# Optimization experiments

Measured on AMD Instinct MI355X. Metric: run time of the kernel, lower is better.

## Reference

```python
import jax, jax.numpy as jnp
import numpy as np
import math

B, S, D, H = 8, 1024, 1024, 16
DH = D // H  # 64


def setup_inputs() -> dict:
    key = jax.random.key(0)
    ks = jax.random.split(key, 10)
    inputs = jax.random.normal(ks[0], (B, S, D), dtype=jnp.float32)
    mask = jax.random.randint(ks[1], (B, S, S), 0, 2) == 1  # bool [B,S,S]
    sc = 1.0 / math.sqrt(D)
    # per-head projection weights stacked: [H, D, DH], biases [H, DH]
    Wq = jax.random.normal(ks[2], (H, D, DH), dtype=jnp.float32) * sc
    bq = jax.random.normal(ks[3], (H, DH), dtype=jnp.float32) * 0.02
    Wk = jax.random.normal(ks[4], (H, D, DH), dtype=jnp.float32) * sc
    bk = jax.random.normal(ks[5], (H, DH), dtype=jnp.float32) * 0.02
    Wv = jax.random.normal(ks[6], (H, D, DH), dtype=jnp.float32) * sc
    bv = jax.random.normal(ks[7], (H, DH), dtype=jnp.float32) * 0.02
    Wo = jax.random.normal(ks[8], (D, D), dtype=jnp.float32) * sc
    bo = jax.random.normal(ks[9], (D,), dtype=jnp.float32) * 0.02
    return {"inputs": inputs, "mask": mask, "Wq": Wq, "bq": bq, "Wk": Wk,
            "bk": bk, "Wv": Wv, "bv": bv, "Wo": Wo, "bo": bo}


def reference(inputs, mask, Wq, bq, Wk, bk, Wv, bv, Wo, bo):
    d_model = inputs.shape[-1]
    scale = 1.0 / jnp.sqrt(jnp.asarray(d_model, inputs.dtype))  # note: sqrt(d_model), as in source
    # batched per-head projections: [B,H,S,DH]
    Q = jnp.einsum('bsd,hde->bhse', inputs, Wq) + bq[None, :, None, :]
    K = jnp.einsum('bsd,hde->bhse', inputs, Wk) + bk[None, :, None, :]
    V = jnp.einsum('bsd,hde->bhse', inputs, Wv) + bv[None, :, None, :]
    scores = jnp.einsum('bhse,bhte->bhst', Q, K) * scale  # [B,H,S,S]
    scores = jnp.where(mask[:, None, :, :], jnp.asarray(-1e9, scores.dtype), scores)
    attn = jax.nn.softmax(scores, axis=-1)
    ctx = jnp.einsum('bhst,bhte->bhse', attn, V)  # [B,H,S,DH]
    # concat heads along last dim (head h -> slice h*DH:(h+1)*DH), matches torch.cat
    bsz, h, s, dh = ctx.shape
    x = ctx.transpose(0, 2, 1, 3).reshape(bsz, s, h * dh)
    return x @ Wo + bo
```

## Files before the change

### kernel.cpp

```cpp
#include <hip/hip_runtime.h>
#include <hip/hip_bf16.h>
#include <stdint.h>


typedef __attribute__((ext_vector_type(8))) short short8;
typedef __attribute__((ext_vector_type(4))) float floatx4;

#define C2S 0.04508422f

__device__ __forceinline__ int swz(int r, int kc) { return r * 8 + (kc ^ (r & 7)); }
__device__ __forceinline__ short8 as_frag(uint4 u) { return __builtin_bit_cast(short8, u); }
__device__ __forceinline__ floatx4 mfma16(short8 a, short8 b, floatx4 c) {
    return __builtin_amdgcn_mfma_f32_16x16x32_bf16(a, b, c, 0, 0, 0);
}
__device__ __forceinline__ unsigned short f2bu(float f) {
    return __builtin_bit_cast(unsigned short, __float2bfloat16(f));
}
__device__ __forceinline__ short f2b(float f) {
    return __builtin_bit_cast(short, __float2bfloat16(f));
}
__device__ __forceinline__ float b2f(short s) {
    return __bfloat162float(__builtin_bit_cast(__hip_bfloat16, s));
}
__device__ __forceinline__ void dma16(const void* g, void* l) {
    __builtin_amdgcn_global_load_lds(
        (const __attribute__((address_space(1))) uint32_t*)g,
        (__attribute__((address_space(3))) uint32_t*)l, 16, 0, 0);
}
__device__ __forceinline__ uint2 pack4(float a, float b, float c, float d) {
    uint2 p;
    p.x = (unsigned)f2bu(a) | ((unsigned)f2bu(b) << 16);
    p.y = (unsigned)f2bu(c) | ((unsigned)f2bu(d) << 16);
    return p;
}

__device__ __forceinline__ void detect_mode(const unsigned* Xw, int* s_is32) {
    if (threadIdx.x < 64) {
        unsigned lo = Xw[threadIdx.x] & 0xFFFFu;
        unsigned e = (lo >> 7) & 0xFFu;
        unsigned long long bal = __ballot(e >= 88u && e <= 150u);
        if (threadIdx.x == 0) *s_is32 = (bal != ~0ull) ? 1 : 0;
    }
    __syncthreads();
}

__device__ __forceinline__ float load_elt(const void* p, size_t idx, int is32) {
    return is32 ? ((const float*)p)[idx]
                : __bfloat162float(((const __hip_bfloat16*)p)[idx]);
}

__global__ __launch_bounds__(256) void prep_all(
    const void* __restrict__ Wq, const void* __restrict__ Wk,
    const void* __restrict__ Wv, const void* __restrict__ Wo,
    const void* __restrict__ bq, const void* __restrict__ bk,
    const void* __restrict__ bv, const void* __restrict__ bo,
    const void* __restrict__ mask_raw, const void* __restrict__ X,
    __hip_bfloat16* __restrict__ WT, __hip_bfloat16* __restrict__ WoT,
    __hip_bfloat16* __restrict__ bc, unsigned long long* __restrict__ bits64,
    __hip_bfloat16* __restrict__ Xb, int do_x)
{
    __shared__ __hip_bfloat16 T[64][72];
    __shared__ int s_is32;
    int blk = blockIdx.x;
    int tid = threadIdx.x;
    const unsigned* Xw = (const unsigned*)X;

    if (blk < 1024) {
        detect_mode(Xw, &s_is32);
        const void* src; size_t src_off;
        __hip_bfloat16* dst;
        int src_ld, dst_ld;
        if (blk < 768) {
            int p = blk >> 8;
            int rem = blk & 255;
            int h = rem >> 4, dt = rem & 15;
            src = (p == 0) ? Wq : (p == 1) ? Wk : Wv;
            src_off = ((size_t)h * 1024 + (size_t)dt * 64) * 64;
            dst = WT + (((size_t)p * 16 + h) * 64) * 1024 + dt * 64;
            src_ld = 64; dst_ld = 1024;
        } else {
            int t = blk - 768;
            int kt = t >> 4, nt = t & 15;
            src = Wo; src_off = (size_t)kt * 64 * 1024 + nt * 64;
            dst = WoT + (size_t)nt * 64 * 1024 + kt * 64;
            src_ld = 1024; dst_ld = 1024;
        }
        #pragma unroll
        for (int i = 0; i < 2; i++) {
            int seg = tid + i * 256;
            int r = seg >> 3, c0 = (seg & 7) * 8;
            if (s_is32) {
                const float* sf = (const float*)src + src_off + (size_t)r * src_ld + c0;
                float4 f0 = *(const float4*)sf;
                float4 f1 = *(const float4*)(sf + 4);
                T[c0 + 0][r] = __float2bfloat16(f0.x);
                T[c0 + 1][r] = __float2bfloat16(f0.y);
                T[c0 + 2][r] = __float2bfloat16(f0.z);
                T[c0 + 3][r] = __float2bfloat16(f0.w);
                T[c0 + 4][r] = __float2bfloat16(f1.x);
                T[c0 + 5][r] = __float2bfloat16(f1.y);
                T[c0 + 6][r] = __float2bfloat16(f1.z);
                T[c0 + 7][r] = __float2bfloat16(f1.w);
            } else {
                const __hip_bfloat16* sh =
                    (const __hip_bfloat16*)src + src_off + (size_t)r * src_ld + c0;
                uint4 u = *(const uint4*)sh;
                short8 s8 = __builtin_bit_cast(short8, u);
                #pragma unroll
                for (int j = 0; j < 8; j++)
                    T[c0 + j][r] = __builtin_bit_cast(__hip_bfloat16, (short)s8[j]);
            }
        }
        __syncthreads();
        #pragma unroll
        for (int i = 0; i < 2; i++) {
            int seg = tid + i * 256;
            int r = seg >> 3, c0 = (seg & 7) * 8;
            *(uint4*)(dst + (size_t)r * dst_ld + c0) = *(const uint4*)(&T[r][c0]);
        }
    } else if (blk == 1024) {
        detect_mode(Xw, &s_is32);
        #pragma unroll
        for (int i = 0; i < 16; i++) {
            int idx = tid + i * 256;
            int which = idx >> 10, j = idx & 1023;
            const void* src = (which == 0) ? bq : (which == 1) ? bk : (which == 2) ? bv : bo;
            float v = load_elt(src, j, s_is32);
            if (which == 0) v *= C2S;
            bc[idx] = __float2bfloat16(v);
        }
    } else if (blk < 2561) {
        int blkL = blk - 1025;
        const int* mi = (const int*)mask_raw;
        const unsigned char* mb = (const unsigned char*)mask_raw;
        int lane = tid & 63;
        bool ok = true;
        #pragma unroll
        for (int i = 0; i < 4; i++) {
            unsigned v = (unsigned)mi[lane * 4 + i];
            if (v > 1u) ok = false;
        }
        bool is_i32 = (__ballot(ok) == ~0ull);
        int gw = (blkL * 256 + tid) >> 6;
        const int NW = 1536 * 4;
        const int NWORDS = (8 * 1024 * 1024) / 64;
        if (is_i32) {
            for (int i = gw; i < NWORDS; i += NW) {
                int mv = mi[(size_t)i * 64 + lane];
                unsigned long long bal = __ballot(mv != 0);
                if (lane == 0) {
                    int bb = i >> 14, q = (i >> 4) & 1023, t = i & 15;
                    bits64[((size_t)bb << 14) + ((size_t)t << 10) + q] = bal;
                }
            }
        } else {
            for (int i = gw; i < NWORDS; i += NW) {
                int mv = mb[(size_t)i * 64 + lane];
                unsigned long long bal = __ballot(mv != 0);
                if (lane == 0) {
                    int bb = i >> 14, q = (i >> 4) & 1023, t = i & 15;
                    bits64[((size_t)bb << 14) + ((size_t)t << 10) + q] = bal;
                }
            }
        }
    } else if (do_x) {
        detect_mode(Xw, &s_is32);
        int blkL = blk - 2561;
        size_t g = ((size_t)blkL * 256 + tid) * 16;
        if (s_is32) {
            const float* Xf = (const float*)X;
            #pragma unroll
            for (int half = 0; half < 2; half++) {
                float4 f0 = *(const float4*)(Xf + g + half * 8);
                float4 f1 = *(const float4*)(Xf + g + half * 8 + 4);
                short8 s;
                s[0] = f2b(f0.x); s[1] = f2b(f0.y); s[2] = f2b(f0.z); s[3] = f2b(f0.w);
                s[4] = f2b(f1.x); s[5] = f2b(f1.y); s[6] = f2b(f1.z); s[7] = f2b(f1.w);
                *(uint4*)(Xb + g + half * 8) = __builtin_bit_cast(uint4, s);
            }
        } else {
            const uint4* Xu = (const uint4*)X;
            *(uint4*)(Xb + g)     = Xu[g / 8];
            *(uint4*)(Xb + g + 8) = Xu[g / 8 + 1];
        }
    }
}

__global__ __launch_bounds__(256, 2) void qkv_gemm_dma(
    const __hip_bfloat16* __restrict__ Xb,
    const __hip_bfloat16* __restrict__ WT,
    const __hip_bfloat16* __restrict__ bc,
    __hip_bfloat16* __restrict__ Q,
    __hip_bfloat16* __restrict__ Ko,
    __hip_bfloat16* __restrict__ Vt)
{
    __shared__ uint4 AsU[256 * 8];
    __shared__ uint4 BsU[128 * 8];
    int tid = threadIdx.x, lane = tid & 63, wave = tid >> 6;
    int quad = lane >> 4, ln = lane & 15;
    int mw = wave & 1, nw = wave >> 1;
    int m0 = blockIdx.x * 256;
    int n0 = blockIdx.y * 128;
    const __hip_bfloat16* Wp = WT + (size_t)n0 * 1024;

    floatx4 acc[8][4];
    #pragma unroll
    for (int i = 0; i < 8; i++)
        #pragma unroll
        for (int j = 0; j < 4; j++) acc[i][j] = (floatx4){0.f, 0.f, 0.f, 0.f};

    for (int k0 = 0; k0 < 1024; k0 += 64) {
        #pragma unroll
        for (int i = 0; i < 8; i++) {
            int r = wave * 64 + i * 8 + (lane >> 3);
            int kc = (lane & 7) ^ (r & 7);
            char* lds = (char*)AsU + (size_t)(wave * 512 + i * 64) * 16;
            dma16(Xb + (size_t)(m0 + r) * 1024 + k0 + kc * 8, lds);
        }
        #pragma unroll
        for (int i = 0; i < 4; i++) {
            int r = wave * 32 + i * 8 + (lane >> 3);
            int kc = (lane & 7) ^ (r & 7);
            char* lds = (char*)BsU + (size_t)(wave * 256 + i * 64) * 16;
            dma16(Wp + (size_t)r * 1024 + k0 + kc * 8, lds);
        }
        __syncthreads();
        #pragma unroll
        for (int kk = 0; kk < 2; kk++) {
            short8 af[8], bf[4];
            #pragma unroll
            for (int mi = 0; mi < 8; mi++)
                af[mi] = as_frag(AsU[swz(mw * 128 + mi * 16 + ln, kk * 4 + quad)]);
            #pragma unroll
            for (int ni = 0; ni < 4; ni++)
                bf[ni] = as_frag(BsU[swz(nw * 64 + ni * 16 + ln, kk * 4 + quad)]);
            #pragma unroll
            for (int mi = 0; mi < 8; mi++)
                #pragma unroll
                for (int ni = 0; ni < 4; ni++)
                    acc[mi][ni] = mfma16(af[mi], bf[ni], acc[mi][ni]);
        }
        __syncthreads();
    }

    int b = m0 >> 10;
    int s0 = m0 & 1023;
    int proj = n0 >> 10;
    if (proj == 2) {
        #pragma unroll
        for (int ni = 0; ni < 4; ni++) {
            int n = n0 + nw * 64 + ni * 16 + ln;
            int h = (n >> 6) & 15, e = n & 63;
            float bval = __bfloat162float(bc[2 * 1024 + (n & 1023)]);
            #pragma unroll
            for (int mi = 0; mi < 8; mi++) {
                int sb = s0 + mw * 128 + mi * 16 + quad * 4;
                uint2 pk = pack4(acc[mi][ni][0] + bval, acc[mi][ni][1] + bval,
                                 acc[mi][ni][2] + bval, acc[mi][ni][3] + bval);
                *(uint2*)(Vt + (((size_t)b * 16 + h) * 64 + e) * 1024 + sb) = pk;
            }
        }
    } else {
        __hip_bfloat16* P = (proj == 0) ? Q : Ko;
        float sc = (proj == 0) ? C2S : 1.f;
        #pragma unroll
        for (int ni = 0; ni < 4; ni++) {
            int n = n0 + nw * 64 + ni * 16 + ln;
            int h = (n >> 6) & 15, e = n & 63;
            float bval = __bfloat162float(bc[proj * 1024 + (n & 1023)]);
            #pragma unroll
            for (int mi = 0; mi < 8; mi++) {
                #pragma unroll
                for (int r = 0; r < 4; r++) {
                    int s = s0 + mw * 128 + mi * 16 + quad * 4 + r;
                    P[(((size_t)b * 16 + h) * 1024 + s) * 64 + e] =
                        __float2bfloat16(acc[mi][ni][r] * sc + bval);
                }
            }
        }
    }
}

__global__ __launch_bounds__(256) void qkv_gemm2(
    const void* __restrict__ Xsrc,
    const __hip_bfloat16* __restrict__ WT,
    const __hip_bfloat16* __restrict__ bc,
    __hip_bfloat16* __restrict__ Q,
    __hip_bfloat16* __restrict__ Ko,
    __hip_bfloat16* __restrict__ Vt)
{
    __shared__ int s_is32;
    detect_mode((const unsigned*)Xsrc, &s_is32);
    __shared__ uint4 AsU[128 * 8];
    __shared__ uint4 BsU[128 * 8];
    int tid = threadIdx.x, lane = tid & 63, wave = tid >> 6;
    int quad = lane >> 4, ln = lane & 15;
    int m0 = blockIdx.x * 128;
    int n0 = blockIdx.y * 128;
    const __hip_bfloat16* Wp = WT + (size_t)n0 * 1024;
    const float* Xf = (const float*)Xsrc;
    const __hip_bfloat16* Xh = (const __hip_bfloat16*)Xsrc;

    floatx4 acc[2][8];
    #pragma unroll
    for (int i = 0; i < 2; i++)
        #pragma unroll
        for (int j = 0; j < 8; j++) acc[i][j] = (floatx4){0.f, 0.f, 0.f, 0.f};

    for (int k0 = 0; k0 < 1024; k0 += 64) {
        if (s_is32) {
            #pragma unroll
            for (int i = 0; i < 4; i++) {
                int id = tid + i * 256;
                int r = id >> 3, kc = id & 7;
                size_t off = (size_t)(m0 + r) * 1024 + k0 + kc * 8;
                float4 f0 = *(const float4*)(Xf + off);
                float4 f1 = *(const float4*)(Xf + off + 4);
                short8 s;
                s[0] = f2b(f0.x); s[1] = f2b(f0.y); s[2] = f2b(f0.z); s[3] = f2b(f0.w);
                s[4] = f2b(f1.x); s[5] = f2b(f1.y); s[6] = f2b(f1.z); s[7] = f2b(f1.w);
                AsU[swz(r, kc)] = __builtin_bit_cast(uint4, s);
            }
        } else {
            #pragma unroll
            for (int i = 0; i < 4; i++) {
                int id = tid + i * 256;
                int r = id >> 3, kc = id & 7;
                AsU[swz(r, kc)] = *(const uint4*)(Xh + (size_t)(m0 + r) * 1024 + k0 + kc * 8);
            }
        }
        #pragma unroll
        for (int i = 0; i < 4; i++) {
            int id = tid + i * 256;
            int r = id >> 3, kc = id & 7;
            BsU[swz(r, kc)] = *(const uint4*)(Wp + (size_t)r * 1024 + k0 + kc * 8);
        }
        __syncthreads();
        #pragma unroll
        for (int kk = 0; kk < 2; kk++) {
            short8 a0 = as_frag(AsU[swz(wave * 32 + ln, kk * 4 + quad)]);
            short8 a1 = as_frag(AsU[swz(wave * 32 + 16 + ln, kk * 4 + quad)]);
            #pragma unroll
            for (int nt = 0; nt < 8; nt++) {
                short8 bf = as_frag(BsU[swz(nt * 16 + ln, kk * 4 + quad)]);
                acc[0][nt] = mfma16(a0, bf, acc[0][nt]);
                acc[1][nt] = mfma16(a1, bf, acc[1][nt]);
            }
        }
        __syncthreads();
    }

    int b = m0 >> 10;
    int s0 = m0 & 1023;
    #pragma unroll
    for (int nt = 0; nt < 8; nt++) {
        int n = n0 + nt * 16 + ln;
        int proj = n >> 10, h = (n >> 6) & 15, e = n & 63;
        float bval = __bfloat162float(bc[proj * 1024 + (n & 1023)]);
        float sc = (proj == 0) ? C2S : 1.f;
        #pragma unroll
        for (int mt = 0; mt < 2; mt++) {
            #pragma unroll
            for (int r = 0; r < 4; r++) {
                int s = s0 + wave * 32 + mt * 16 + quad * 4 + r;
                float v = acc[mt][nt][r] * sc + bval;
                if (proj == 2) {
                    Vt[(((size_t)b * 16 + h) * 64 + e) * 1024 + s] = __float2bfloat16(v);
                } else {
                    __hip_bfloat16* P = (proj == 0) ? Q : Ko;
                    P[(((size_t)b * 16 + h) * 1024 + s) * 64 + e] = __float2bfloat16(v);
                }
            }
        }
    }
}

__global__ __launch_bounds__(512, 4) void attn(
    const __hip_bfloat16* __restrict__ Q,
    const __hip_bfloat16* __restrict__ K,
    const __hip_bfloat16* __restrict__ Vt,
    const unsigned long long* __restrict__ bits,
    __hip_bfloat16* __restrict__ ctx)
{
    __shared__ uint4 KsU[2 * 512];
    __shared__ uint4 VsU[2 * 512];
    __shared__ uint4 PsU[8 * 256];

    int tid = threadIdx.x, lane = tid & 63, w = tid >> 6;
    int quad = lane >> 4, ln = lane & 15;
    int bh = blockIdx.x;
    int q0 = blockIdx.y * 256;
    int b = bh >> 4, h = bh & 15;
    const __hip_bfloat16* Qp = Q + (size_t)bh * 1024 * 64;
    const __hip_bfloat16* Kp = K + (size_t)bh * 1024 * 64;
    const __hip_bfloat16* Vp = Vt + (size_t)bh * 64 * 1024;
    const unsigned long long* bp = bits + (size_t)b * 16 * 1024;

    short8 qf[2][2];
    #pragma unroll
    for (int g = 0; g < 2; g++)
        #pragma unroll
        for (int kk = 0; kk < 2; kk++)
            qf[g][kk] = as_frag(*(const uint4*)(
                Qp + (size_t)(q0 + w * 32 + g * 16 + ln) * 64 + kk * 32 + quad * 8));

    int r8 = lane >> 3;
    int kc = (lane & 7) ^ r8;

    floatx4 acc_o[2][4];
    #pragma unroll
    for (int g = 0; g < 2; g++)
        #pragma unroll
        for (int i = 0; i < 4; i++) acc_o[g][i] = (floatx4){0.f, 0.f, 0.f, 0.f};
    float lsum[2] = {0.f, 0.f};
    __hip_bfloat16* Pw = (__hip_bfloat16*)&PsU[w * 256];

    for (int t0 = 0; t0 < 1024; t0 += 128) {
        __syncthreads();
        int t64b = t0 >> 6;
        unsigned long long m00 = bp[((size_t)t64b << 10) + q0 + w * 32 + ln];
        unsigned long long m01 = bp[((size_t)t64b << 10) + q0 + w * 32 + 16 + ln];
        unsigned long long m10 = bp[((size_t)(t64b + 1) << 10) + q0 + w * 32 + ln];
        unsigned long long m11 = bp[((size_t)(t64b + 1) << 10) + q0 + w * 32 + 16 + ln];
        #pragma unroll
        for (int i = 0; i < 2; i++) {
            int tK = t0 + i * 64 + w * 8 + r8;
            dma16(Kp + (size_t)tK * 64 + kc * 8,
                  (char*)KsU + (size_t)(i * 512 + w * 64) * 16);
            int e = w * 8 + r8;
            dma16(Vp + (size_t)e * 1024 + t0 + i * 64 + kc * 8,
                  (char*)VsU + (size_t)(i * 512 + w * 64) * 16);
        }
        __syncthreads();

        #pragma unroll
        for (int s = 0; s < 2; s++) {
            unsigned long long mcur0 = s ? m10 : m00;
            unsigned long long mcur1 = s ? m11 : m01;
            const uint4* Ks = KsU + s * 512;
            const uint4* Vs = VsU + s * 512;

            floatx4 st[2][4];
            #pragma unroll
            for (int g = 0; g < 2; g++)
                #pragma unroll
                for (int i = 0; i < 4; i++) st[g][i] = (floatx4){0.f, 0.f, 0.f, 0.f};
            __builtin_amdgcn_s_setprio(1);
            #pragma unroll
            for (int kk = 0; kk < 2; kk++) {
                #pragma unroll
                for (int tt = 0; tt < 4; tt++) {
                    short8 kf = as_frag(Ks[swz(tt * 16 + ln, kk * 4 + quad)]);
                    st[0][tt] = mfma16(kf, qf[0][kk], st[0][tt]);
                    st[1][tt] = mfma16(kf, qf[1][kk], st[1][tt]);
                }
            }
            __builtin_amdgcn_s_setprio(0);

            #pragma unroll
            for (int g = 0; g < 2; g++) {
                int qloc = g * 16 + ln;
                unsigned long long msh = (g ? mcur1 : mcur0) >> (quad * 4);
                #pragma unroll
                for (int tt = 0; tt < 4; tt++) {
                    unsigned mb = (unsigned)(msh >> (tt * 16)) & 0xFu;
                    float pe0 = (mb & 1u) ? 0.f : __builtin_amdgcn_exp2f(st[g][tt][0]);
                    float pe1 = (mb & 2u) ? 0.f : __builtin_amdgcn_exp2f(st[g][tt][1]);
                    float pe2 = (mb & 4u) ? 0.f : __builtin_amdgcn_exp2f(st[g][tt][2]);
                    float pe3 = (mb & 8u) ? 0.f : __builtin_amdgcn_exp2f(st[g][tt][3]);
                    lsum[g] += (pe0 + pe1) + (pe2 + pe3);
                    int kcp = tt * 2 + (quad >> 1);
                    int off = qloc * 64 + (kcp ^ (qloc & 7)) * 8 + (quad & 1) * 4;
                    *(uint2*)(Pw + off) = pack4(pe0, pe1, pe2, pe3);
                }
            }

            __builtin_amdgcn_s_setprio(1);
            #pragma unroll
            for (int kk = 0; kk < 2; kk++) {
                short8 pf0 = as_frag(PsU[w * 256 + swz(0 * 16 + ln, kk * 4 + quad)]);
                short8 pf1 = as_frag(PsU[w * 256 + swz(1 * 16 + ln, kk * 4 + quad)]);
                #pragma unroll
                for (int et = 0; et < 4; et++) {
                    short8 vf = as_frag(Vs[swz(et * 16 + ln, kk * 4 + quad)]);
                    acc_o[0][et] = mfma16(vf, pf0, acc_o[0][et]);
                    acc_o[1][et] = mfma16(vf, pf1, acc_o[1][et]);
                }
            }
            __builtin_amdgcn_s_setprio(0);
        }
    }

    #pragma unroll
    for (int g = 0; g < 2; g++) {
        lsum[g] += __shfl_xor(lsum[g], 16, 64);
        lsum[g] += __shfl_xor(lsum[g], 32, 64);
    }

    #pragma unroll
    for (int g = 0; g < 2; g++) {
        float inv = 1.f / fmaxf(lsum[g], 1e-20f);
        int s = q0 + w * 32 + g * 16 + ln;
        __hip_bfloat16* crow = ctx + ((size_t)b * 1024 + s) * 1024 + h * 64 + quad * 4;
        #pragma unroll
        for (int et = 0; et < 4; et++) {
            uint2 pk = pack4(acc_o[g][et][0] * inv, acc_o[g][et][1] * inv,
                             acc_o[g][et][2] * inv, acc_o[g][et][3] * inv);
            *(uint2*)(crow + et * 16) = pk;
        }
    }
}

__global__ __launch_bounds__(256) void out_gemm_dma(
    const __hip_bfloat16* __restrict__ Cx,
    const __hip_bfloat16* __restrict__ WoT,
    const __hip_bfloat16* __restrict__ bc,
    const unsigned* __restrict__ Xw,
    void* __restrict__ dout,
    int direct)
{
    __shared__ int s_is32;
    detect_mode(Xw, &s_is32);
    __shared__ uint4 AsU[128 * 8];
    __shared__ uint4 BsU[128 * 8];
    int tid = threadIdx.x, lane = tid & 63, wave = tid >> 6;
    int quad = lane >> 4, ln = lane & 15;
    int mw = wave & 1, nw = wave >> 1;
    int m0 = blockIdx.x * 128;
    int n0 = blockIdx.y * 128;

    floatx4 acc[4][4];
    #pragma unroll
    for (int i = 0; i < 4; i++)
        #pragma unroll
        for (int j = 0; j < 4; j++) acc[i][j] = (floatx4){0.f, 0.f, 0.f, 0.f};

    for (int k0 = 0; k0 < 1024; k0 += 64) {
        #pragma unroll
        for (int i = 0; i < 4; i++) {
            int r = wave * 32 + i * 8 + (lane >> 3);
            int kc = (lane & 7) ^ (r & 7);
            char* ldsA = (char*)AsU + (size_t)(wave * 256 + i * 64) * 16;
            char* ldsB = (char*)BsU + (size_t)(wave * 256 + i * 64) * 16;
            dma16(Cx + (size_t)(m0 + r) * 1024 + k0 + kc * 8, ldsA);
            dma16(WoT + (size_t)(n0 + r) * 1024 + k0 + kc * 8, ldsB);
        }
        __syncthreads();
        #pragma unroll
        for (int kk = 0; kk < 2; kk++) {
            short8 af[4], bf[4];
            #pragma unroll
            for (int mi = 0; mi < 4; mi++)
                af[mi] = as_frag(AsU[swz(mw * 64 + mi * 16 + ln, kk * 4 + quad)]);
            #pragma unroll
            for (int ni = 0; ni < 4; ni++)
                bf[ni] = as_frag(BsU[swz(nw * 64 + ni * 16 + ln, kk * 4 + quad)]);
            #pragma unroll
            for (int mi = 0; mi < 4; mi++)
                #pragma unroll
                for (int ni = 0; ni < 4; ni++)
                    acc[mi][ni] = mfma16(af[mi], bf[ni], acc[mi][ni]);
        }
        __syncthreads();
    }

    const __hip_bfloat16* bo = bc + 3 * 1024;
    #pragma unroll
    for (int ni = 0; ni < 4; ni++) {
        int n = n0 + nw * 64 + ni * 16 + ln;
        float bval = __bfloat162float(bo[n]);
        #pragma unroll
        for (int mi = 0; mi < 4; mi++) {
            #pragma unroll
            for (int r = 0; r < 4; r++) {
                int m = m0 + mw * 64 + mi * 16 + quad * 4 + r;
                float v = acc[mi][ni][r] + bval;
                if (direct && s_is32) ((float*)dout)[(size_t)m * 1024 + n] = v;
                else ((__hip_bfloat16*)dout)[(size_t)m * 1024 + n] = __float2bfloat16(v);
            }
        }
    }
}

__global__ __launch_bounds__(256) void emit_out(
    const __hip_bfloat16* __restrict__ Fo, const unsigned* __restrict__ Xw,
    void* __restrict__ dout)
{
    __shared__ int s_is32;
    detect_mode(Xw, &s_is32);
    size_t g = (size_t)blockIdx.x * 256 + threadIdx.x;
    uint4 u = *(const uint4*)(Fo + g * 8);
    if (s_is32) {
        short8 s = __builtin_bit_cast(short8, u);
        float4 f0, f1;
        f0.x = b2f(s[0]); f0.y = b2f(s[1]); f0.z = b2f(s[2]); f0.w = b2f(s[3]);
        f1.x = b2f(s[4]); f1.y = b2f(s[5]); f1.z = b2f(s[6]); f1.w = b2f(s[7]);
        *(float4*)((float*)dout + g * 8) = f0;
        *(float4*)((float*)dout + g * 8 + 4) = f1;
    } else {
        *(uint4*)((__hip_bfloat16*)dout + g * 8) = u;
    }
}

extern "C" void kernel_launch(void* const* d_in, const int* in_sizes, int n_in,
                              void* d_out, int out_size, void* d_ws, size_t ws_size,
                              hipStream_t stream) {
    const void* X  = d_in[0];
    const void* mk = d_in[1];
    const void* Wq = d_in[2];
    const void* bq = d_in[3];
    const void* Wk = d_in[4];
    const void* bk = d_in[5];
    const void* Wv = d_in[6];
    const void* bv = d_in[7];
    const void* Wo = d_in[8];
    const void* bo = d_in[9];
    const unsigned* Xw = (const unsigned*)X;

    char* ws = (char*)d_ws;
    __hip_bfloat16*     WT   = (__hip_bfloat16*)(ws);
    __hip_bfloat16*     WoT  = (__hip_bfloat16*)(ws + ((size_t)6 << 20));
    unsigned long long* bits = (unsigned long long*)(ws + ((size_t)8 << 20));
    __hip_bfloat16*     bc   = (__hip_bfloat16*)(ws + ((size_t)9 << 20));
    __hip_bfloat16*     Xb   = (__hip_bfloat16*)(ws + ((size_t)10 << 20));
    __hip_bfloat16*     Qb   = (__hip_bfloat16*)(ws + ((size_t)26 << 20));
    __hip_bfloat16*     Kb   = (__hip_bfloat16*)(ws + ((size_t)42 << 20));
    __hip_bfloat16*     Vtb  = (__hip_bfloat16*)(ws + ((size_t)58 << 20));

    bool bigws = ws_size >= ((size_t)74 << 20);

    hipLaunchKernelGGL(prep_all, dim3(4609), dim3(256), 0, stream,
                       Wq, Wk, Wv, Wo, bq, bk, bv, bo, mk, X,
                       WT, WoT, bc, bits, Xb, bigws ? 1 : 0);

    if (bigws) {
        __hip_bfloat16* Cx = Xb;
        hipLaunchKernelGGL(qkv_gemm_dma, dim3(32, 24), dim3(256), 0, stream,
                           Xb, WT, bc, Qb, Kb, Vtb);
        hipLaunchKernelGGL(attn, dim3(128, 4), dim3(512), 0, stream,
                           Qb, Kb, Vtb, bits, Cx);
        hipLaunchKernelGGL(out_gemm_dma, dim3(64, 8), dim3(256), 0, stream,
                           Cx, WoT, bc, Xw, d_out, 1);
    } else {
        __hip_bfloat16* Cx = (__hip_bfloat16*)d_out;
        __hip_bfloat16* Fo = Qb;
        hipLaunchKernelGGL(qkv_gemm2, dim3(64, 24), dim3(256), 0, stream,
                           X, WT, bc, Qb, Kb, Vtb);
        hipLaunchKernelGGL(attn, dim3(128, 4), dim3(512), 0, stream,
                           Qb, Kb, Vtb, bits, Cx);
        hipLaunchKernelGGL(out_gemm_dma, dim3(64, 8), dim3(256), 0, stream,
                           Cx, WoT, bc, Xw, (void*)Fo, 0);
        hipLaunchKernelGGL(emit_out, dim3(4096), dim3(256), 0, stream,
                           Fo, Xw, d_out);
    }
}
```

Before: 289.6 us.

## Pipeline QKV GEMM with double-buffered async loads and 256x256 tiles

Rewrites the QKV projection GEMM to use 512-thread blocks computing 256x256 tiles. The K dimension is split into 32-wide half-stages that are double-buffered in LDS. Async global-to-LDS copies for upcoming stages are issued between MFMA phases, gated by explicit vmcnt waits and raw barriers, and s_setprio raises the MFMA issue priority. The goal is to overlap memory traffic with matrix math and halve the number of B-tile reloads. In exchange the kernel uses 128KB of LDS, which lowers occupancy, and relies on hand-placed wait counts being correct.

```diff
diff --git a/kernel.cpp b/kernel.cpp
--- a/kernel.cpp
+++ b/kernel.cpp
@@ -186,7 +186,48 @@
     }
 }
 
-__global__ __launch_bounds__(256, 2) void qkv_gemm_dma(
+#define VM6 asm volatile("s_waitcnt vmcnt(6)" ::: "memory")
+#define VM0 asm volatile("s_waitcnt vmcnt(0)" ::: "memory")
+#define FENCE asm volatile("" ::: "memory")
+
+#define QPH(BUF, KK, MH, LOADB, STAGE_STMT, WAIT_STMT)                          \
+  {                                                                             \
+    const int base_ = ((BUF) * 2 + (KK)) * 1024;                                \
+    short8 af0 = as_frag(AsU[base_ + (mw * 128 + ((MH) * 4 + 0) * 16 + ln) * 4 + rslot]); \
+    short8 af1 = as_frag(AsU[base_ + (mw * 128 + ((MH) * 4 + 1) * 16 + ln) * 4 + rslot]); \
+    short8 af2 = as_frag(AsU[base_ + (mw * 128 + ((MH) * 4 + 2) * 16 + ln) * 4 + rslot]); \
+    short8 af3 = as_frag(AsU[base_ + (mw * 128 + ((MH) * 4 + 3) * 16 + ln) * 4 + rslot]); \
+    if (LOADB) {                                                                \
+      bf[0] = as_frag(BsU[base_ + (nw * 64 + 0 * 16 + ln) * 4 + rslot]);        \
+      bf[1] = as_frag(BsU[base_ + (nw * 64 + 1 * 16 + ln) * 4 + rslot]);        \
+      bf[2] = as_frag(BsU[base_ + (nw * 64 + 2 * 16 + ln) * 4 + rslot]);        \
+      bf[3] = as_frag(BsU[base_ + (nw * 64 + 3 * 16 + ln) * 4 + rslot]);        \
+    }                                                                           \
+    STAGE_STMT;                                                                 \
+    FENCE; __builtin_amdgcn_s_barrier(); FENCE;                                 \
+    __builtin_amdgcn_s_setprio(1);                                              \
+    acc[(MH) * 4 + 0][0] = mfma16(af0, bf[0], acc[(MH) * 4 + 0][0]);            \
+    acc[(MH) * 4 + 0][1] = mfma16(af0, bf[1], acc[(MH) * 4 + 0][1]);            \
+    acc[(MH) * 4 + 0][2] = mfma16(af0, bf[2], acc[(MH) * 4 + 0][2]);            \
+    acc[(MH) * 4 + 0][3] = mfma16(af0, bf[3], acc[(MH) * 4 + 0][3]);            \
+    acc[(MH) * 4 + 1][0] = mfma16(af1, bf[0], acc[(MH) * 4 + 1][0]);            \
+    acc[(MH) * 4 + 1][1] = mfma16(af1, bf[1], acc[(MH) * 4 + 1][1]);            \
+    acc[(MH) * 4 + 1][2] = mfma16(af1, bf[2], acc[(MH) * 4 + 1][2]);            \
+    acc[(MH) * 4 + 1][3] = mfma16(af1, bf[3], acc[(MH) * 4 + 1][3]);            \
+    acc[(MH) * 4 + 2][0] = mfma16(af2, bf[0], acc[(MH) * 4 + 2][0]);            \
+    acc[(MH) * 4 + 2][1] = mfma16(af2, bf[1], acc[(MH) * 4 + 2][1]);            \
+    acc[(MH) * 4 + 2][2] = mfma16(af2, bf[2], acc[(MH) * 4 + 2][2]);            \
+    acc[(MH) * 4 + 2][3] = mfma16(af2, bf[3], acc[(MH) * 4 + 2][3]);            \
+    acc[(MH) * 4 + 3][0] = mfma16(af3, bf[0], acc[(MH) * 4 + 3][0]);            \
+    acc[(MH) * 4 + 3][1] = mfma16(af3, bf[1], acc[(MH) * 4 + 3][1]);            \
+    acc[(MH) * 4 + 3][2] = mfma16(af3, bf[2], acc[(MH) * 4 + 3][2]);            \
+    acc[(MH) * 4 + 3][3] = mfma16(af3, bf[3], acc[(MH) * 4 + 3][3]);            \
+    __builtin_amdgcn_s_setprio(0);                                              \
+    WAIT_STMT;                                                                  \
+    FENCE; __builtin_amdgcn_s_barrier(); FENCE;                                 \
+  }
+
+__global__ __launch_bounds__(512, 2) void qkv_gemm_dma(
     const __hip_bfloat16* __restrict__ Xb,
     const __hip_bfloat16* __restrict__ WT,
     const __hip_bfloat16* __restrict__ bc,
@@ -194,53 +235,63 @@
     __hip_bfloat16* __restrict__ Ko,
     __hip_bfloat16* __restrict__ Vt)
 {
-    __shared__ uint4 AsU[256 * 8];
-    __shared__ uint4 BsU[128 * 8];
-    int tid = threadIdx.x, lane = tid & 63, wave = tid >> 6;
+    __shared__ uint4 AsU[4096];
+    __shared__ uint4 BsU[4096];
+    int tid = threadIdx.x, lane = tid & 63, w = tid >> 6;
     int quad = lane >> 4, ln = lane & 15;
-    int mw = wave & 1, nw = wave >> 1;
+    int mw = w & 1, nw = w >> 1;
     int m0 = blockIdx.x * 256;
-    int n0 = blockIdx.y * 128;
+    int n0 = blockIdx.y * 256;
     const __hip_bfloat16* Wp = WT + (size_t)n0 * 1024;
 
+    int l2 = lane >> 2;
+    int kcS = (lane & 3) ^ (l2 & 3);
+    int rslot = quad ^ (ln & 3);
+
     floatx4 acc[8][4];
     #pragma unroll
     for (int i = 0; i < 8; i++)
         #pragma unroll
         for (int j = 0; j < 4; j++) acc[i][j] = (floatx4){0.f, 0.f, 0.f, 0.f};
 
-    for (int k0 = 0; k0 < 1024; k0 += 64) {
-        #pragma unroll
-        for (int i = 0; i < 8; i++) {
-            int r = wave * 64 + i * 8 + (lane >> 3);
-            int kc = (lane & 7) ^ (r & 7);
-            char* lds = (char*)AsU + (size_t)(wave * 512 + i * 64) * 16;
-            dma16(Xb + (size_t)(m0 + r) * 1024 + k0 + kc * 8, lds);
-        }
-        #pragma unroll
-        for (int i = 0; i < 4; i++) {
-            int r = wave * 32 + i * 8 + (lane >> 3);
-            int kc = (lane & 7) ^ (r & 7);
-            char* lds = (char*)BsU + (size_t)(wave * 256 + i * 64) * 16;
-            dma16(Wp + (size_t)r * 1024 + k0 + kc * 8, lds);
-        }
-        __syncthreads();
-        #pragma unroll
-        for (int kk = 0; kk < 2; kk++) {
-            short8 af[8], bf[4];
-            #pragma unroll
-            for (int mi = 0; mi < 8; mi++)
-                af[mi] = as_frag(AsU[swz(mw * 128 + mi * 16 + ln, kk * 4 + quad)]);
-            #pragma unroll
-            for (int ni = 0; ni < 4; ni++)
-                bf[ni] = as_frag(BsU[swz(nw * 64 + ni * 16 + ln, kk * 4 + quad)]);
-            #pragma unroll
-            for (int mi = 0; mi < 8; mi++)
-                #pragma unroll
-                for (int ni = 0; ni < 4; ni++)
-                    acc[mi][ni] = mfma16(af[mi], bf[ni], acc[mi][ni]);
-        }
-        __syncthreads();
+    auto stA = [&](int kt, int kh) {
+        int kh2 = (kt & 1) * 2 + kh;
+        #pragma unroll
+        for (int j = 0; j < 2; j++) {
+            int r = (w * 2 + j) * 16 + l2;
+            dma16(Xb + (size_t)(m0 + r) * 1024 + kt * 64 + kh * 32 + kcS * 8,
+                  (char*)AsU + (size_t)(kh2 * 1024 + (w * 2 + j) * 64) * 16);
+        }
+    };
+    auto stB = [&](int kt, int kh) {
+        int kh2 = (kt & 1) * 2 + kh;
+        #pragma unroll
+        for (int j = 0; j < 2; j++) {
+            int r = (w * 2 + j) * 16 + l2;
+            dma16(Wp + (size_t)r * 1024 + kt * 64 + kh * 32 + kcS * 8,
+                  (char*)BsU + (size_t)(kh2 * 1024 + (w * 2 + j) * 64) * 16);
+        }
+    };
+
+    stB(0, 0); stA(0, 0); stB(0, 1); stA(0, 1);
+    stB(1, 0); stA(1, 0); stB(1, 1);
+    VM6;
+    FENCE; __builtin_amdgcn_s_barrier(); FENCE;
+
+    short8 bf[4];
+    for (int it = 0; it < 8; it++) {
+        int T = 2 * it;
+        bool more = (it < 7);
+        QPH(0, 0, 0, 1, { stA(T + 1, 1); },              {})
+        QPH(0, 0, 1, 0, { if (more) stB(T + 2, 0); },    {})
+        QPH(0, 1, 0, 1, { if (more) stA(T + 2, 0); },    {})
+        QPH(0, 1, 1, 0, { if (more) stB(T + 2, 1); },
+            { if (more) { VM6; } else { VM0; } })
+        QPH(1, 0, 0, 1, { if (more) stA(T + 2, 1); },    {})
+        QPH(1, 0, 1, 0, { if (more) stB(T + 3, 0); },    {})
+        QPH(1, 1, 0, 1, { if (more) stA(T + 3, 0); },    {})
+        QPH(1, 1, 1, 0, { if (more) stB(T + 3, 1); },
+            { if (more) { VM6; } })
     }
 
     int b = m0 >> 10;
@@ -342,9 +393,9 @@
             short8 a1 = as_frag(AsU[swz(wave * 32 + 16 + ln, kk * 4 + quad)]);
             #pragma unroll
             for (int nt = 0; nt < 8; nt++) {
-                short8 bf = as_frag(BsU[swz(nt * 16 + ln, kk * 4 + quad)]);
-                acc[0][nt] = mfma16(a0, bf, acc[0][nt]);
-                acc[1][nt] = mfma16(a1, bf, acc[1][nt]);
+                short8 bfr = as_frag(BsU[swz(nt * 16 + ln, kk * 4 + quad)]);
+                acc[0][nt] = mfma16(a0, bfr, acc[0][nt]);
+                acc[1][nt] = mfma16(a1, bfr, acc[1][nt]);
             }
         }
         __syncthreads();
@@ -548,18 +599,18 @@
         __syncthreads();
         #pragma unroll
         for (int kk = 0; kk < 2; kk++) {
-            short8 af[4], bf[4];
+            short8 af[4], bfr[4];
             #pragma unroll
             for (int mi = 0; mi < 4; mi++)
                 af[mi] = as_frag(AsU[swz(mw * 64 + mi * 16 + ln, kk * 4 + quad)]);
             #pragma unroll
             for (int ni = 0; ni < 4; ni++)
-                bf[ni] = as_frag(BsU[swz(nw * 64 + ni * 16 + ln, kk * 4 + quad)]);
+                bfr[ni] = as_frag(BsU[swz(nw * 64 + ni * 16 + ln, kk * 4 + quad)]);
             #pragma unroll
             for (int mi = 0; mi < 4; mi++)
                 #pragma unroll
                 for (int ni = 0; ni < 4; ni++)
-                    acc[mi][ni] = mfma16(af[mi], bf[ni], acc[mi][ni]);
+                    acc[mi][ni] = mfma16(af[mi], bfr[ni], acc[mi][ni]);
         }
         __syncthreads();
     }
@@ -635,7 +686,7 @@
 
     if (bigws) {
         __hip_bfloat16* Cx = Xb;
-        hipLaunchKernelGGL(qkv_gemm_dma, dim3(32, 24), dim3(256), 0, stream,
+        hipLaunchKernelGGL(qkv_gemm_dma, dim3(32, 12), dim3(512), 0, stream,
                            Xb, WT, bc, Qb, Kb, Vtb);
         hipLaunchKernelGGL(attn, dim3(128, 4), dim3(512), 0, stream,
                            Qb, Kb, Vtb, bits, Cx);
```

Result: slower. 303.8 us (+4.9%).
